# Kernel tuning notes

Measured on AMD Instinct MI355X. Metric: run time of the kernel, lower is better.

The kernel has to match this reference:

```python
import jax, jax.numpy as jnp
import numpy as np

N = 10000
E = 160000
NEG_SLOPE = 0.2
BN_EPS = 1e-5


def _gat_conv(x, W, a_src, a_dst, b, src, dst, n, heads):
    # PyG GATConv, concat=False (mean over heads), shared lin for src/dst.
    H = heads
    C = W.shape[1] // H
    h = (x @ W).reshape(n, H, C)                       # (N,H,C)
    e_s = jnp.einsum('nhc,hc->nh', h, a_src)           # (N,H)
    e_d = jnp.einsum('nhc,hc->nh', h, a_dst)
    alpha = jax.nn.leaky_relu(e_s[src] + e_d[dst], NEG_SLOPE)   # (E',H)
    amax = jax.ops.segment_max(alpha, dst, num_segments=n)       # per-dst softmax
    ex = jnp.exp(alpha - amax[dst])
    denom = jax.ops.segment_sum(ex, dst, num_segments=n)
    w = ex / (denom[dst] + 1e-16)
    out = jax.ops.segment_sum(h[src] * w[:, :, None], dst, num_segments=n)  # (N,H,C)
    return out.mean(axis=1) + b


def _bn(x, g, b):
    mu = x.mean(axis=0)
    var = x.var(axis=0)  # biased, as torch BN training forward
    return (x - mu) * jax.lax.rsqrt(var + BN_EPS) * g + b


def setup_inputs() -> dict:
    key = jax.random.key(0)
    ks = jax.random.split(key, 32)
    d = {}
    d['x'] = jax.random.normal(ks[0], (N, 64), jnp.float32)
    d['edge_index'] = jax.random.randint(ks[1], (2, E), 0, N, jnp.int64)
    s = lambda k, shape, fan: jax.random.normal(k, shape, jnp.float32) * (1.0 / np.sqrt(fan))
    d['Wp'] = s(ks[2], (64, 128), 64); d['bp'] = jnp.zeros((128,), jnp.float32)
    # conv0: 8 heads, per-head 128
    d['W0'] = s(ks[3], (128, 8 * 128), 128); d['as0'] = s(ks[4], (8, 128), 128)
    d['ad0'] = s(ks[5], (8, 128), 128); d['b0'] = jnp.zeros((128,), jnp.float32)
    d['g0'] = jnp.ones((128,), jnp.float32); d['be0'] = jnp.zeros((128,), jnp.float32)
    # conv1: same shape
    d['W1'] = s(ks[6], (128, 8 * 128), 128); d['as1'] = s(ks[7], (8, 128), 128)
    d['ad1'] = s(ks[8], (8, 128), 128); d['b1'] = jnp.zeros((128,), jnp.float32)
    d['g1'] = jnp.ones((128,), jnp.float32); d['be1'] = jnp.zeros((128,), jnp.float32)
    # conv2: 1 head, out 64
    d['W2'] = s(ks[9], (128, 64), 128); d['as2'] = s(ks[10], (1, 64), 64)
    d['ad2'] = s(ks[11], (1, 64), 64); d['b2'] = jnp.zeros((64,), jnp.float32)
    d['g2'] = jnp.ones((64,), jnp.float32); d['be2'] = jnp.zeros((64,), jnp.float32)
    # residual projection for layer 2 (128 -> 64)
    d['Wr'] = s(ks[12], (128, 64), 128); d['br'] = jnp.zeros((64,), jnp.float32)
    return d


def reference(x, edge_index, Wp, bp, W0, as0, ad0, b0, g0, be0,
              W1, as1, ad1, b1, g1, be1, W2, as2, ad2, b2, g2, be2, Wr, br):
    n = x.shape[0]
    loops = jnp.arange(n, dtype=edge_index.dtype)
    src = jnp.concatenate([edge_index[0], loops])  # add_self_loops=True
    dst = jnp.concatenate([edge_index[1], loops])
    h = x @ Wp + bp
    # layer 0 (8 heads, identity residual)
    hr = h
    h = jax.nn.elu(_bn(_gat_conv(h, W0, as0, ad0, b0, src, dst, n, 8), g0, be0)) + hr
    # layer 1
    hr = h
    h = jax.nn.elu(_bn(_gat_conv(h, W1, as1, ad1, b1, src, dst, n, 8), g1, be1)) + hr
    # layer 2 (1 head, linear residual 128->64)
    hr = h @ Wr + br
    h = jax.nn.elu(_bn(_gat_conv(h, W2, as2, ad2, b2, src, dst, n, 1), g2, be2)) + hr
    return h
```

## Files before the change

kernel.cpp:

```cpp
#include <hip/hip_runtime.h>
#include <hip/hip_bf16.h>
#include <cstdint>
#include <cstddef>

#define TPB 256

typedef __attribute__((ext_vector_type(8))) short bf16x8;
typedef __attribute__((ext_vector_type(8))) unsigned short ushort8;
typedef __attribute__((ext_vector_type(4))) float f32x4;

static __device__ __forceinline__ float bf2f(unsigned short u) {
  union { unsigned int i; float f; } c;
  c.i = ((unsigned int)u) << 16;
  return c.f;
}
static __device__ __forceinline__ unsigned short f2us(float v) {
  __hip_bfloat16 b = __float2bfloat16(v);
  return *(unsigned short*)&b;
}

__global__ void detect_kernel(const unsigned int* __restrict__ w, int* __restrict__ flag) {
  __shared__ int any32;
  if (threadIdx.x == 0) any32 = 0;
  __syncthreads();
  for (int i = threadIdx.x; i < 1024; i += TPB)
    if (w[2 * i + 1] != 0u) any32 = 1;
  __syncthreads();
  if (threadIdx.x == 0) *flag = any32;
}

__global__ void decode_kernel(const void* __restrict__ raw, const int* __restrict__ flag,
                              int* __restrict__ src, int* __restrict__ dst, int E, int n) {
  int i = blockIdx.x * TPB + threadIdx.x;
  int tot = E + n;
  if (i >= tot) return;
  if (i < E) {
    if (*flag) {
      const int* p = (const int*)raw;
      src[i] = p[i];
      dst[i] = p[E + i];
    } else {
      const long long* p = (const long long*)raw;
      src[i] = (int)p[i];
      dst[i] = (int)p[E + i];
    }
  } else {
    src[i] = i - E;
    dst[i] = i - E;
  }
}

__global__ void count_kernel(const int* __restrict__ dst, int* __restrict__ counts, int etot) {
  int i = blockIdx.x * TPB + threadIdx.x;
  if (i < etot) atomicAdd(&counts[dst[i]], 1);
}

__global__ void scan_kernel(const int* __restrict__ counts, int* __restrict__ row_ptr, int n) {
  __shared__ int part[TPB];
  int tid = threadIdx.x;
  int chunk = (n + TPB - 1) / TPB;
  int begin = tid * chunk;
  int end = begin + chunk; if (end > n) end = n;
  int s = 0;
  for (int i = begin; i < end && i < n; i++) s += counts[i];
  part[tid] = s;
  __syncthreads();
  for (int off = 1; off < TPB; off <<= 1) {
    int v = (tid >= off) ? part[tid - off] : 0;
    __syncthreads();
    part[tid] += v;
    __syncthreads();
  }
  int base = (tid == 0) ? 0 : part[tid - 1];
  for (int i = begin; i < end && i < n; i++) { row_ptr[i] = base; base += counts[i]; }
  if (tid == TPB - 1) row_ptr[n] = base;
}

__global__ void fill_kernel(const int* __restrict__ src, const int* __restrict__ dst,
                            const int* __restrict__ row_ptr, int* __restrict__ fill,
                            int* __restrict__ sorted_src, int etot) {
  int i = blockIdx.x * TPB + threadIdx.x;
  if (i >= etot) return;
  int d = dst[i];
  int pos = row_ptr[d] + atomicAdd(&fill[d], 1);
  sorted_src[pos] = src[i];
}

__global__ void f32_to_bf16_kernel(const float* __restrict__ in, __hip_bfloat16* __restrict__ out, int n) {
  int i = blockIdx.x * TPB + threadIdx.x;
  if (i < n) out[i] = __float2bfloat16(in[i]);
}

__global__ void f32_to_bf16_T_kernel(const float* __restrict__ in, __hip_bfloat16* __restrict__ out,
                                     int K, int N) {
  __shared__ float tile[32][33];
  const int k0 = blockIdx.x * 32, n0 = blockIdx.y * 32;
  const int tx = threadIdx.x & 31, ty = threadIdx.x >> 5;
  for (int r = ty; r < 32; r += 8) {
    int k = k0 + r, n = n0 + tx;
    tile[r][tx] = (k < K && n < N) ? in[(size_t)k * N + n] : 0.f;
  }
  __syncthreads();
  for (int r = ty; r < 32; r += 8) {
    int n = n0 + r, k = k0 + tx;
    if (n < N && k < K) out[(size_t)n * K + k] = __float2bfloat16(tile[tx][r]);
  }
}

__global__ __launch_bounds__(256) void gemm_bf16t_kernel(
    const short* __restrict__ A, const short* __restrict__ Bt,
    const float* __restrict__ bias, float* __restrict__ C,
    __hip_bfloat16* __restrict__ Cb, int M, int Ncols, int K,
    const float* __restrict__ asrc, const float* __restrict__ adst,
    float* __restrict__ es_out, float* __restrict__ ed_out, int H, int hshift) {
  __shared__ short As[64][40];
  __shared__ short Bs[128][40];

  const int tid = threadIdx.x;
  const int lane = tid & 63;
  const int w = tid >> 6;
  const int bm = blockIdx.x * 64;
  const int bn = blockIdx.y * 128;

  f32x4 acc[8];
#pragma unroll
  for (int nt = 0; nt < 8; nt++) acc[nt] = (f32x4){0.f, 0.f, 0.f, 0.f};

  const int arow = tid >> 2;
  const int akk = (tid & 3) << 3;
  const int brow = tid >> 1;
  const int bkk = (tid & 1) << 4;

  for (int k0 = 0; k0 < K; k0 += 32) {
    {
      int gr = bm + arow;
      if (gr < M) {
        *(bf16x8*)&As[arow][akk] = *(const bf16x8*)&A[(size_t)gr * K + k0 + akk];
      } else {
        bf16x8 z = {0, 0, 0, 0, 0, 0, 0, 0};
        *(bf16x8*)&As[arow][akk] = z;
      }
    }
    {
      int gbn = bn + brow;
      if (gbn < Ncols) {
        const short* bp = &Bt[(size_t)gbn * K + k0 + bkk];
        *(bf16x8*)&Bs[brow][bkk]     = *(const bf16x8*)bp;
        *(bf16x8*)&Bs[brow][bkk + 8] = *(const bf16x8*)(bp + 8);
      } else {
        bf16x8 z = {0, 0, 0, 0, 0, 0, 0, 0};
        *(bf16x8*)&Bs[brow][bkk] = z;
        *(bf16x8*)&Bs[brow][bkk + 8] = z;
      }
    }
    __syncthreads();

    bf16x8 a = *(const bf16x8*)&As[w * 16 + (lane & 15)][(lane >> 4) * 8];
#pragma unroll
    for (int nt = 0; nt < 8; nt++) {
      bf16x8 b = *(const bf16x8*)&Bs[nt * 16 + (lane & 15)][(lane >> 4) * 8];
      acc[nt] = __builtin_amdgcn_mfma_f32_16x16x32_bf16(a, b, acc[nt], 0, 0, 0);
    }
    __syncthreads();
  }

  float p1[4] = {0.f, 0.f, 0.f, 0.f};
  float p2[4] = {0.f, 0.f, 0.f, 0.f};

#pragma unroll
  for (int nt = 0; nt < 8; nt++) {
    int gc = bn + nt * 16 + (lane & 15);
    if (gc >= Ncols) continue;
    float bv = bias ? bias[gc] : 0.f;
    float asv = es_out ? asrc[gc] : 0.f;
    float adv = es_out ? adst[gc] : 0.f;
#pragma unroll
    for (int q = 0; q < 4; q++) {
      int gr = bm + w * 16 + (lane >> 4) * 4 + q;
      if (gr < M) {
        float val = acc[nt][q] + bv;
        if (C) C[(size_t)gr * Ncols + gc] = val;
        if (Cb) Cb[(size_t)gr * Ncols + gc] = __float2bfloat16(val);
        p1[q] += val * asv;
        p2[q] += val * adv;
      }
    }
  }

  if (es_out) {
    const int head = bn >> hshift;
#pragma unroll
    for (int q = 0; q < 4; q++) {
      float s1 = p1[q], s2 = p2[q];
      s1 += __shfl_xor(s1, 1); s2 += __shfl_xor(s2, 1);
      s1 += __shfl_xor(s1, 2); s2 += __shfl_xor(s2, 2);
      s1 += __shfl_xor(s1, 4); s2 += __shfl_xor(s2, 4);
      s1 += __shfl_xor(s1, 8); s2 += __shfl_xor(s2, 8);
      int gr = bm + w * 16 + (lane >> 4) * 4 + q;
      if ((lane & 15) == 0 && gr < M) {
        es_out[(size_t)gr * H + head] = s1;
        ed_out[(size_t)gr * H + head] = s2;
      }
    }
  }
}

__global__ __launch_bounds__(256) void gat_weights_kernel(
    const int* __restrict__ row_ptr, const int* __restrict__ srcs,
    const float* __restrict__ es, const float* __restrict__ ed,
    float* __restrict__ wbuf, int etot, int n) {
  const int wave = threadIdx.x >> 6, lane = threadIdx.x & 63;
  const int v = blockIdx.x * 4 + wave;
  if (v >= n) return;
  const int begin = row_ptr[v], deg = row_ptr[v + 1] - begin;
  const int eh = lane & 7, ee = lane >> 3;
  const float edv = ed[(size_t)v * 8 + eh];

  if (deg <= 64) {
    float a[8];
#pragma unroll
    for (int b = 0; b < 8; b++) {
      a[b] = -1e30f;
      int e = b * 8 + ee;
      if (e < deg) {
        int s = srcs[begin + e];
        float t = es[(size_t)s * 8 + eh] + edv;
        a[b] = t > 0.f ? t : 0.2f * t;
      }
    }
    float m = a[0];
#pragma unroll
    for (int b = 1; b < 8; b++) m = fmaxf(m, a[b]);
    m = fmaxf(m, __shfl_xor(m, 8));
    m = fmaxf(m, __shfl_xor(m, 16));
    m = fmaxf(m, __shfl_xor(m, 32));
    float dsum = 0.f;
#pragma unroll
    for (int b = 0; b < 8; b++) { a[b] = __expf(a[b] - m); dsum += a[b]; }
    dsum += __shfl_xor(dsum, 8);
    dsum += __shfl_xor(dsum, 16);
    dsum += __shfl_xor(dsum, 32);
    const float invd = 1.0f / (dsum + 1e-16f);
#pragma unroll
    for (int b = 0; b < 8; b++) {
      int e = b * 8 + ee;
      if (e < deg) wbuf[(size_t)eh * etot + begin + e] = a[b] * invd;
    }
  } else {
    float m = -1e30f;
    for (int e = ee; e < deg; e += 8) {
      int s = srcs[begin + e];
      float t = es[(size_t)s * 8 + eh] + edv;
      t = t > 0.f ? t : 0.2f * t;
      m = fmaxf(m, t);
    }
    m = fmaxf(m, __shfl_xor(m, 8));
    m = fmaxf(m, __shfl_xor(m, 16));
    m = fmaxf(m, __shfl_xor(m, 32));
    float dsum = 0.f;
    for (int e = ee; e < deg; e += 8) {
      int s = srcs[begin + e];
      float t = es[(size_t)s * 8 + eh] + edv;
      t = t > 0.f ? t : 0.2f * t;
      dsum += __expf(t - m);
    }
    dsum += __shfl_xor(dsum, 8);
    dsum += __shfl_xor(dsum, 16);
    dsum += __shfl_xor(dsum, 32);
    const float invd = 1.0f / (dsum + 1e-16f);
    for (int e = ee; e < deg; e += 8) {
      int s = srcs[begin + e];
      float t = es[(size_t)s * 8 + eh] + edv;
      t = t > 0.f ? t : 0.2f * t;
      wbuf[(size_t)eh * etot + begin + e] = __expf(t - m) * invd;
    }
  }
}

__global__ __launch_bounds__(256) void gat_gather_head_kernel(
    const int* __restrict__ row_ptr, const int* __restrict__ srcs,
    const unsigned short* __restrict__ gb, const float* __restrict__ wbuf,
    unsigned short* __restrict__ partial, int etot, int n, int nb) {
  const int h = blockIdx.x & 7;
  const int nblk = blockIdx.x >> 3;
  const int wave = threadIdx.x >> 6, lane = threadIdx.x & 63;

  __shared__ float wlds[4][64];
  __shared__ int slds[4][64];

  const int per = (n + nb - 1) / nb;
  const int v1 = min((nblk + 1) * per, n);
  const float* wb = wbuf + (size_t)h * etot;
  const unsigned short* gsl = gb + h * 128;
  unsigned short* pout = partial + (size_t)h * n * 128;
  const int g = lane >> 4;
  const int c8 = (lane & 15) * 8;

  for (int v = nblk * per + wave; v < v1; v += 4) {
    const int begin = row_ptr[v];
    const int deg = row_ptr[v + 1] - begin;
    float acc[8];
#pragma unroll
    for (int k = 0; k < 8; k++) acc[k] = 0.f;

    for (int base = 0; base < deg; base += 64) {
      const int cnt = min(64, deg - base);
      int sv = 0; float wv = 0.f;
      if (lane < cnt) {
        sv = srcs[begin + base + lane];
        wv = wb[begin + base + lane];
      }
      slds[wave][lane] = sv;
      wlds[wave][lane] = wv;
      const int npad = (cnt + 15) & ~15;
      for (int j0 = 0; j0 < npad; j0 += 16) {
        int s0 = slds[wave][j0 + g];
        int s1 = slds[wave][j0 + 4 + g];
        int s2 = slds[wave][j0 + 8 + g];
        int s3 = slds[wave][j0 + 12 + g];
        float w0 = wlds[wave][j0 + g];
        float w1 = wlds[wave][j0 + 4 + g];
        float w2 = wlds[wave][j0 + 8 + g];
        float w3 = wlds[wave][j0 + 12 + g];
        ushort8 u0 = *(const ushort8*)&gsl[(size_t)s0 * 1024 + c8];
        ushort8 u1 = *(const ushort8*)&gsl[(size_t)s1 * 1024 + c8];
        ushort8 u2 = *(const ushort8*)&gsl[(size_t)s2 * 1024 + c8];
        ushort8 u3 = *(const ushort8*)&gsl[(size_t)s3 * 1024 + c8];
#pragma unroll
        for (int k = 0; k < 8; k++) {
          acc[k] += w0 * bf2f(u0[k]) + w1 * bf2f(u1[k])
                  + w2 * bf2f(u2[k]) + w3 * bf2f(u3[k]);
        }
      }
    }

#pragma unroll
    for (int k = 0; k < 8; k++) {
      acc[k] += __shfl_xor(acc[k], 16);
      acc[k] += __shfl_xor(acc[k], 32);
    }
    if (lane < 16) {
      unsigned int o[4];
#pragma unroll
      for (int k = 0; k < 4; k++)
        o[k] = (unsigned int)f2us(acc[2 * k]) | ((unsigned int)f2us(acc[2 * k + 1]) << 16);
      *(uint4*)&pout[(size_t)v * 128 + c8] = *(uint4*)o;
    }
  }
}

__global__ __launch_bounds__(256) void gat_reduce_bn_kernel(
    const unsigned short* __restrict__ partial, const float* __restrict__ bias,
    float* __restrict__ out, float* __restrict__ sums, int n) {
  const int t = threadIdx.x;
  const int stride = gridDim.x * TPB;
  float s0 = 0.f, q0 = 0.f, s1 = 0.f, q1 = 0.f;
  for (int idx = blockIdx.x * TPB + t; idx < n * 64; idx += stride) {
    int v = idx >> 6, c = (idx & 63) * 2;
    float sx = 0.f, sy = 0.f;
#pragma unroll
    for (int h = 0; h < 8; h++) {
      unsigned int u = *(const unsigned int*)&partial[(size_t)h * n * 128 + (size_t)v * 128 + c];
      sx += bf2f((unsigned short)u);
      sy += bf2f((unsigned short)(u >> 16));
    }
    float x0 = sx * 0.125f + bias[c];
    float x1 = sy * 0.125f + bias[c + 1];
    out[(size_t)v * 128 + c]     = x0;
    out[(size_t)v * 128 + c + 1] = x1;
    s0 += x0; q0 += x0 * x0;
    s1 += x1; q1 += x1 * x1;
  }
  __shared__ float ls0[TPB], lq0[TPB], ls1[TPB], lq1[TPB];
  ls0[t] = s0; lq0[t] = q0; ls1[t] = s1; lq1[t] = q1;
  __syncthreads();
  if (t < 64) {
    float S0 = ls0[t] + ls0[t + 64] + ls0[t + 128] + ls0[t + 192];
    float Q0 = lq0[t] + lq0[t + 64] + lq0[t + 128] + lq0[t + 192];
    float S1 = ls1[t] + ls1[t + 64] + ls1[t + 128] + ls1[t + 192];
    float Q1 = lq1[t] + lq1[t + 64] + lq1[t + 128] + lq1[t + 192];
    int c = t * 2;
    atomicAdd(&sums[c], S0);
    atomicAdd(&sums[128 + c], Q0);
    atomicAdd(&sums[c + 1], S1);
    atomicAdd(&sums[128 + c + 1], Q1);
  }
}

__global__ __launch_bounds__(256) void gat_aggregate1_kernel(
    const int* __restrict__ row_ptr, const int* __restrict__ srcs,
    const float* __restrict__ g, const float* __restrict__ es,
    const float* __restrict__ ed, const float* __restrict__ bias,
    float* __restrict__ out, int n) {
  const int wave = threadIdx.x >> 6;
  const int lane = threadIdx.x & 63;
  const int v = blockIdx.x * 4 + wave;

  __shared__ float wlds[4][64];
  __shared__ int slds[4][64];

  if (v >= n) return;

  const int begin = row_ptr[v];
  const int deg = row_ptr[v + 1] - begin;
  const float edv = ed[v];

  float acc = 0.f;

  if (deg <= 64) {
    float a = -1e30f;
    int s = 0;
    if (lane < deg) {
      s = srcs[begin + lane];
      float t = es[s] + edv;
      a = t > 0.f ? t : 0.2f * t;
    }
    float m = a;
#pragma unroll
    for (int off = 32; off > 0; off >>= 1) m = fmaxf(m, __shfl_xor(m, off));
    float p = __expf(a - m);
    float dsum = p;
#pragma unroll
    for (int off = 32; off > 0; off >>= 1) dsum += __shfl_xor(dsum, off);
    const float invd = 1.0f / (dsum + 1e-16f);
    wlds[wave][lane] = p * invd;
    slds[wave][lane] = s;

    const int npad = (deg + 7) & ~7;
    for (int j0 = 0; j0 < npad; j0 += 8) {
      float w0 = wlds[wave][j0 + 0], w1 = wlds[wave][j0 + 1];
      float w2 = wlds[wave][j0 + 2], w3 = wlds[wave][j0 + 3];
      float w4 = wlds[wave][j0 + 4], w5 = wlds[wave][j0 + 5];
      float w6 = wlds[wave][j0 + 6], w7 = wlds[wave][j0 + 7];
      int s0 = slds[wave][j0 + 0], s1 = slds[wave][j0 + 1];
      int s2 = slds[wave][j0 + 2], s3 = slds[wave][j0 + 3];
      int s4 = slds[wave][j0 + 4], s5 = slds[wave][j0 + 5];
      int s6 = slds[wave][j0 + 6], s7 = slds[wave][j0 + 7];
      float f0 = g[(size_t)s0 * 64 + lane];
      float f1 = g[(size_t)s1 * 64 + lane];
      float f2 = g[(size_t)s2 * 64 + lane];
      float f3 = g[(size_t)s3 * 64 + lane];
      float f4 = g[(size_t)s4 * 64 + lane];
      float f5 = g[(size_t)s5 * 64 + lane];
      float f6 = g[(size_t)s6 * 64 + lane];
      float f7 = g[(size_t)s7 * 64 + lane];
      acc += (w0 * f0 + w1 * f1) + (w2 * f2 + w3 * f3)
           + (w4 * f4 + w5 * f5) + (w6 * f6 + w7 * f7);
    }
  } else {
    float pm = -1e30f;
    for (int j = lane; j < deg; j += 64) {
      float a = es[srcs[begin + j]] + edv;
      a = a > 0.f ? a : 0.2f * a;
      pm = fmaxf(pm, a);
    }
#pragma unroll
    for (int off = 32; off > 0; off >>= 1) pm = fmaxf(pm, __shfl_xor(pm, off));
    float ps = 0.f;
    for (int j = lane; j < deg; j += 64) {
      float a = es[srcs[begin + j]] + edv;
      a = a > 0.f ? a : 0.2f * a;
      ps += __expf(a - pm);
    }
#pragma unroll
    for (int off = 32; off > 0; off >>= 1) ps += __shfl_xor(ps, off);
    const float invd = 1.0f / (ps + 1e-16f);

    for (int base = 0; base < deg; base += 64) {
      int cnt = min(64, deg - base);
      float wv = 0.f; int s = 0;
      if (lane < cnt) {
        s = srcs[begin + base + lane];
        float a = es[s] + edv;
        a = a > 0.f ? a : 0.2f * a;
        wv = __expf(a - pm) * invd;
      }
      wlds[wave][lane] = wv;
      slds[wave][lane] = s;
      const int npad = (cnt + 7) & ~7;
      for (int j0 = 0; j0 < npad; j0 += 8) {
        float w0 = wlds[wave][j0 + 0], w1 = wlds[wave][j0 + 1];
        float w2 = wlds[wave][j0 + 2], w3 = wlds[wave][j0 + 3];
        float w4 = wlds[wave][j0 + 4], w5 = wlds[wave][j0 + 5];
        float w6 = wlds[wave][j0 + 6], w7 = wlds[wave][j0 + 7];
        int s0 = slds[wave][j0 + 0], s1 = slds[wave][j0 + 1];
        int s2 = slds[wave][j0 + 2], s3 = slds[wave][j0 + 3];
        int s4 = slds[wave][j0 + 4], s5 = slds[wave][j0 + 5];
        int s6 = slds[wave][j0 + 6], s7 = slds[wave][j0 + 7];
        float f0 = g[(size_t)s0 * 64 + lane];
        float f1 = g[(size_t)s1 * 64 + lane];
        float f2 = g[(size_t)s2 * 64 + lane];
        float f3 = g[(size_t)s3 * 64 + lane];
        float f4 = g[(size_t)s4 * 64 + lane];
        float f5 = g[(size_t)s5 * 64 + lane];
        float f6 = g[(size_t)s6 * 64 + lane];
        float f7 = g[(size_t)s7 * 64 + lane];
        acc += (w0 * f0 + w1 * f1) + (w2 * f2 + w3 * f3)
             + (w4 * f4 + w5 * f5) + (w6 * f6 + w7 * f7);
      }
    }
  }
  out[(size_t)v * 64 + lane] = acc + bias[lane];
}

template <int C>
__global__ void bn_stats_kernel(const float* __restrict__ x, int n, float* __restrict__ sums) {
  constexpr int T = 256;
  constexpr int RPI = T / C;
  constexpr int ITER = 8;
  constexpr int ROWS = RPI * ITER;
  int c = threadIdx.x % C;
  int r0 = threadIdx.x / C;
  int rowBase = blockIdx.x * ROWS;
  float s = 0.f, q = 0.f;
  for (int it = 0; it < ITER; ++it) {
    int r = rowBase + it * RPI + r0;
    if (r < n) {
      float v = x[(size_t)r * C + c];
      s += v; q += v * v;
    }
  }
  __shared__ float ls[T], lq[T];
  ls[threadIdx.x] = s; lq[threadIdx.x] = q;
  __syncthreads();
  if (threadIdx.x < C) {
    float ts = 0.f, tq = 0.f;
    for (int r = 0; r < RPI; ++r) { ts += ls[c + r * C]; tq += lq[c + r * C]; }
    atomicAdd(&sums[c], ts);
    atomicAdd(&sums[C + c], tq);
  }
}

template <int C>
__global__ void bn_elu_res_kernel(const float* __restrict__ x, const float* __restrict__ sums,
                                  const float* __restrict__ gamma, const float* __restrict__ beta,
                                  const float* __restrict__ res, float* __restrict__ out,
                                  __hip_bfloat16* __restrict__ outb, int n) {
  int i = blockIdx.x * TPB + threadIdx.x;
  if (i >= n * C) return;
  int c = i % C;
  float inv_n = 1.0f / (float)n;
  float mu = sums[c] * inv_n;
  float var = sums[C + c] * inv_n - mu * mu;
  float y = (x[i] - mu) * rsqrtf(var + 1e-5f) * gamma[c] + beta[c];
  y = y > 0.f ? y : expm1f(y);
  y += res[i];
  out[i] = y;
  if (outb) outb[i] = __float2bfloat16(y);
}

extern "C" void kernel_launch(void* const* d_in, const int* in_sizes, int n_in,
                              void* d_out, int out_size, void* d_ws, size_t ws_size,
                              hipStream_t stream) {
  const float* x   = (const float*)d_in[0];
  const void*  ei  = d_in[1];
  const float* Wp  = (const float*)d_in[2];
  const float* bp  = (const float*)d_in[3];
  const float* W0  = (const float*)d_in[4];
  const float* as0 = (const float*)d_in[5];
  const float* ad0 = (const float*)d_in[6];
  const float* b0  = (const float*)d_in[7];
  const float* g0  = (const float*)d_in[8];
  const float* be0 = (const float*)d_in[9];
  const float* W1  = (const float*)d_in[10];
  const float* as1 = (const float*)d_in[11];
  const float* ad1 = (const float*)d_in[12];
  const float* b1  = (const float*)d_in[13];
  const float* g1  = (const float*)d_in[14];
  const float* be1 = (const float*)d_in[15];
  const float* W2  = (const float*)d_in[16];
  const float* as2 = (const float*)d_in[17];
  const float* ad2 = (const float*)d_in[18];
  const float* b2  = (const float*)d_in[19];
  const float* g2  = (const float*)d_in[20];
  const float* be2 = (const float*)d_in[21];
  const float* Wr  = (const float*)d_in[22];
  const float* br  = (const float*)d_in[23];

  const int N = in_sizes[0] / 64;
  const int E = in_sizes[1] / 2;
  const int ETOT = E + N;

  char* wsp = (char*)d_ws;
  size_t off = 0;
  auto alloc = [&](size_t bytes) -> void* {
    void* p = wsp + off;
    off += (bytes + 255) & ~(size_t)255;
    return p;
  };
  int*   flag    = (int*)alloc(4);
  int*   e_src   = (int*)alloc((size_t)ETOT * 4);
  int*   e_dst   = (int*)alloc((size_t)ETOT * 4);
  int*   counts  = (int*)alloc((size_t)N * 4);
  int*   fillc   = (int*)alloc((size_t)N * 4);
  int*   row_ptr = (int*)alloc((size_t)(N + 1) * 4);
  int*   s_src   = (int*)alloc((size_t)ETOT * 4);
  float* hA      = (float*)alloc((size_t)N * 128 * 4);
  float* hB      = (float*)alloc((size_t)N * 128 * 4);
  float* gat     = (float*)alloc((size_t)N * 128 * 4);
  float* es      = (float*)alloc((size_t)N * 8 * 4);
  float* ed      = (float*)alloc((size_t)N * 8 * 4);
  float* bnsum   = (float*)alloc(2 * 128 * 4);
  float* wbuf    = (float*)alloc((size_t)ETOT * 8 * 4);
  __hip_bfloat16* gbufb = (__hip_bfloat16*)alloc((size_t)N * 1024 * 2);
  float* gbuf    = (float*)gbufb;
  unsigned short* partial = (unsigned short*)alloc((size_t)N * 1024 * 2);
  __hip_bfloat16* xb  = (__hip_bfloat16*)alloc((size_t)N * 64 * 2);
  __hip_bfloat16* hAb = (__hip_bfloat16*)alloc((size_t)N * 128 * 2);
  __hip_bfloat16* hBb = (__hip_bfloat16*)alloc((size_t)N * 128 * 2);
  __hip_bfloat16* WpT = (__hip_bfloat16*)alloc((size_t)128 * 64 * 2);
  __hip_bfloat16* W0T = (__hip_bfloat16*)alloc((size_t)1024 * 128 * 2);
  __hip_bfloat16* W1T = (__hip_bfloat16*)alloc((size_t)1024 * 128 * 2);
  __hip_bfloat16* W2T = (__hip_bfloat16*)alloc((size_t)64 * 128 * 2);
  __hip_bfloat16* WrT = (__hip_bfloat16*)alloc((size_t)64 * 128 * 2);

  const int egrid = (ETOT + TPB - 1) / TPB;
  const int mgrid = (N + 63) / 64;
  const int NB = 512;
  auto cgrid = [](int n) { return (n + TPB - 1) / TPB; };

  detect_kernel<<<1, TPB, 0, stream>>>((const unsigned int*)ei, flag);
  decode_kernel<<<egrid, TPB, 0, stream>>>(ei, flag, e_src, e_dst, E, N);
  hipMemsetAsync(counts, 0, (size_t)N * 4, stream);
  hipMemsetAsync(fillc, 0, (size_t)N * 4, stream);
  count_kernel<<<egrid, TPB, 0, stream>>>(e_dst, counts, ETOT);
  scan_kernel<<<1, TPB, 0, stream>>>(counts, row_ptr, N);
  fill_kernel<<<egrid, TPB, 0, stream>>>(e_src, e_dst, row_ptr, fillc, s_src, ETOT);

  f32_to_bf16_kernel<<<cgrid(N * 64), TPB, 0, stream>>>(x, xb, N * 64);
  f32_to_bf16_T_kernel<<<dim3(2, 4), 256, 0, stream>>>(Wp, WpT, 64, 128);
  f32_to_bf16_T_kernel<<<dim3(4, 32), 256, 0, stream>>>(W0, W0T, 128, 1024);
  f32_to_bf16_T_kernel<<<dim3(4, 32), 256, 0, stream>>>(W1, W1T, 128, 1024);
  f32_to_bf16_T_kernel<<<dim3(4, 2), 256, 0, stream>>>(W2, W2T, 128, 64);
  f32_to_bf16_T_kernel<<<dim3(4, 2), 256, 0, stream>>>(Wr, WrT, 128, 64);

  gemm_bf16t_kernel<<<dim3(mgrid, 1), 256, 0, stream>>>(
      (const short*)xb, (const short*)WpT, bp, hA, hAb, N, 128, 64,
      nullptr, nullptr, nullptr, nullptr, 1, 7);

  gemm_bf16t_kernel<<<dim3(mgrid, 8), 256, 0, stream>>>(
      (const short*)hAb, (const short*)W0T, nullptr, nullptr, gbufb, N, 1024, 128,
      as0, ad0, es, ed, 8, 7);
  gat_weights_kernel<<<(N + 3) / 4, 256, 0, stream>>>(row_ptr, s_src, es, ed, wbuf, ETOT, N);
  gat_gather_head_kernel<<<8 * NB, 256, 0, stream>>>(
      row_ptr, s_src, (const unsigned short*)gbufb, wbuf, partial, ETOT, N, NB);
  hipMemsetAsync(bnsum, 0, 2 * 128 * 4, stream);
  gat_reduce_bn_kernel<<<512, 256, 0, stream>>>(partial, b0, gat, bnsum, N);
  bn_elu_res_kernel<128><<<cgrid(N * 128), TPB, 0, stream>>>(gat, bnsum, g0, be0, hA, hB, hBb, N);

  gemm_bf16t_kernel<<<dim3(mgrid, 8), 256, 0, stream>>>(
      (const short*)hBb, (const short*)W1T, nullptr, nullptr, gbufb, N, 1024, 128,
      as1, ad1, es, ed, 8, 7);
  gat_weights_kernel<<<(N + 3) / 4, 256, 0, stream>>>(row_ptr, s_src, es, ed, wbuf, ETOT, N);
  gat_gather_head_kernel<<<8 * NB, 256, 0, stream>>>(
      row_ptr, s_src, (const unsigned short*)gbufb, wbuf, partial, ETOT, N, NB);
  hipMemsetAsync(bnsum, 0, 2 * 128 * 4, stream);
  gat_reduce_bn_kernel<<<512, 256, 0, stream>>>(partial, b1, gat, bnsum, N);
  bn_elu_res_kernel<128><<<cgrid(N * 128), TPB, 0, stream>>>(gat, bnsum, g1, be1, hB, hA, hAb, N);

  gemm_bf16t_kernel<<<dim3(mgrid, 1), 256, 0, stream>>>(
      (const short*)hAb, (const short*)WrT, br, hB, nullptr, N, 64, 128,
      nullptr, nullptr, nullptr, nullptr, 1, 7);
  gemm_bf16t_kernel<<<dim3(mgrid, 1), 256, 0, stream>>>(
      (const short*)hAb, (const short*)W2T, nullptr, gbuf, nullptr, N, 64, 128,
      as2, ad2, es, ed, 1, 6);
  gat_aggregate1_kernel<<<(N + 3) / 4, 256, 0, stream>>>(row_ptr, s_src, gbuf, es, ed, b2, gat, N);
  hipMemsetAsync(bnsum, 0, 2 * 64 * 4, stream);
  bn_stats_kernel<64><<<(N + 31) / 32, 256, 0, stream>>>(gat, N, bnsum);
  bn_elu_res_kernel<64><<<cgrid(N * 64), TPB, 0, stream>>>(gat, bnsum, g2, be2, hB, (float*)d_out, nullptr, N);
}
```

Baseline: 312.4 us.

## Fuse GAT softmax into gather, merge small kernels and layer-2 GEMMs

The separate attention-weight kernel is removed: per-edge softmax weights are now computed inside the head gather kernel, so the edge-by-head weight buffer is never written to or read back from global memory. Setup kernels are merged: detect, memset and count fold into prep and decode-count kernels, and the five weight-transpose launches become one. The layer-2 residual projection and conv2 GEMM are combined into a single 128-wide GEMM, BN stats are folded into the aggregate kernel, and the bnsum memsets move into the GEMM. The softmax logits are recomputed in the gather for each edge, and in the high-degree path they are recomputed twice.

```diff
diff --git a/kernel.cpp b/kernel.cpp
--- a/kernel.cpp
+++ b/kernel.cpp
@@ -19,40 +19,41 @@
   return *(unsigned short*)&b;
 }
 
-__global__ void detect_kernel(const unsigned int* __restrict__ w, int* __restrict__ flag) {
-  __shared__ int any32;
-  if (threadIdx.x == 0) any32 = 0;
-  __syncthreads();
-  for (int i = threadIdx.x; i < 1024; i += TPB)
-    if (w[2 * i + 1] != 0u) any32 = 1;
-  __syncthreads();
-  if (threadIdx.x == 0) *flag = any32;
-}
-
-__global__ void decode_kernel(const void* __restrict__ raw, const int* __restrict__ flag,
-                              int* __restrict__ src, int* __restrict__ dst, int E, int n) {
+__global__ void prep_kernel(const unsigned int* __restrict__ ei, int* __restrict__ flag,
+                            int* __restrict__ counts, int* __restrict__ fillc, int n) {
+  int i = blockIdx.x * TPB + threadIdx.x;
+  if (i < n) { counts[i] = 0; fillc[i] = 0; }
+  if (blockIdx.x == 0) {
+    __shared__ int any32;
+    if (threadIdx.x == 0) any32 = 0;
+    __syncthreads();
+    for (int k = threadIdx.x; k < 1024; k += TPB)
+      if (ei[2 * k + 1] != 0u) any32 = 1;
+    __syncthreads();
+    if (threadIdx.x == 0) *flag = any32;
+  }
+}
+
+__global__ void decode_count_kernel(const void* __restrict__ raw, const int* __restrict__ flag,
+                                    int* __restrict__ src, int* __restrict__ dst,
+                                    int* __restrict__ counts, int E, int n) {
   int i = blockIdx.x * TPB + threadIdx.x;
   int tot = E + n;
   if (i >= tot) return;
+  int s, d;
   if (i < E) {
     if (*flag) {
       const int* p = (const int*)raw;
-      src[i] = p[i];
-      dst[i] = p[E + i];
+      s = p[i]; d = p[E + i];
     } else {
       const long long* p = (const long long*)raw;
-      src[i] = (int)p[i];
-      dst[i] = (int)p[E + i];
+      s = (int)p[i]; d = (int)p[E + i];
     }
   } else {
-    src[i] = i - E;
-    dst[i] = i - E;
-  }
-}
-
-__global__ void count_kernel(const int* __restrict__ dst, int* __restrict__ counts, int etot) {
-  int i = blockIdx.x * TPB + threadIdx.x;
-  if (i < etot) atomicAdd(&counts[dst[i]], 1);
+    s = i - E; d = i - E;
+  }
+  src[i] = s; dst[i] = d;
+  atomicAdd(&counts[d], 1);
 }
 
 __global__ void scan_kernel(const int* __restrict__ counts, int* __restrict__ row_ptr, int n) {
@@ -91,19 +92,43 @@
   if (i < n) out[i] = __float2bfloat16(in[i]);
 }
 
-__global__ void f32_to_bf16_T_kernel(const float* __restrict__ in, __hip_bfloat16* __restrict__ out,
-                                     int K, int N) {
+__global__ void convert_weights_kernel(
+    const float* __restrict__ Wp, const float* __restrict__ W0,
+    const float* __restrict__ W1, const float* __restrict__ W2,
+    const float* __restrict__ Wr, const float* __restrict__ as2,
+    const float* __restrict__ ad2, const float* __restrict__ br,
+    __hip_bfloat16* __restrict__ WpT, __hip_bfloat16* __restrict__ W0T,
+    __hip_bfloat16* __restrict__ W1T, __hip_bfloat16* __restrict__ WrW2T,
+    float* __restrict__ asrc_c, float* __restrict__ adst_c, float* __restrict__ bias_c) {
+  const int b = blockIdx.x;
+  if (b == 280) {
+    int t = threadIdx.x;
+    if (t < 128) {
+      asrc_c[t] = (t < 64) ? 0.f : as2[t - 64];
+      adst_c[t] = (t < 64) ? 0.f : ad2[t - 64];
+      bias_c[t] = (t < 64) ? br[t] : 0.f;
+    }
+    return;
+  }
+  const float* src; __hip_bfloat16* dst; int K, N, t;
+  if (b < 8)        { src = Wp; dst = WpT; K = 64;  N = 128;  t = b; }
+  else if (b < 136) { src = W0; dst = W0T; K = 128; N = 1024; t = b - 8; }
+  else if (b < 264) { src = W1; dst = W1T; K = 128; N = 1024; t = b - 136; }
+  else if (b < 272) { src = W2; dst = WrW2T + 64 * 128; K = 128; N = 64; t = b - 264; }
+  else              { src = Wr; dst = WrW2T;            K = 128; N = 64; t = b - 272; }
+
   __shared__ float tile[32][33];
-  const int k0 = blockIdx.x * 32, n0 = blockIdx.y * 32;
+  const int kt = (K + 31) / 32;
+  const int k0 = (t % kt) * 32, n0 = (t / kt) * 32;
   const int tx = threadIdx.x & 31, ty = threadIdx.x >> 5;
   for (int r = ty; r < 32; r += 8) {
     int k = k0 + r, n = n0 + tx;
-    tile[r][tx] = (k < K && n < N) ? in[(size_t)k * N + n] : 0.f;
+    tile[r][tx] = (k < K && n < N) ? src[(size_t)k * N + n] : 0.f;
   }
   __syncthreads();
   for (int r = ty; r < 32; r += 8) {
     int n = n0 + r, k = k0 + tx;
-    if (n < N && k < K) out[(size_t)n * K + k] = __float2bfloat16(tile[tx][r]);
+    if (n < N && k < K) dst[(size_t)n * K + k] = __float2bfloat16(tile[tx][r]);
   }
 }
 
@@ -112,11 +137,14 @@
     const float* __restrict__ bias, float* __restrict__ C,
     __hip_bfloat16* __restrict__ Cb, int M, int Ncols, int K,
     const float* __restrict__ asrc, const float* __restrict__ adst,
-    float* __restrict__ es_out, float* __restrict__ ed_out, int H, int hshift) {
+    float* __restrict__ es_out, float* __restrict__ ed_out, int H, int hshift,
+    float* __restrict__ bn_zero, int bn_len) {
   __shared__ short As[64][40];
   __shared__ short Bs[128][40];
 
   const int tid = threadIdx.x;
+  if (bn_zero && blockIdx.x == 0 && blockIdx.y == 0 && tid < bn_len) bn_zero[tid] = 0.f;
+
   const int lane = tid & 63;
   const int w = tid >> 6;
   const int bm = blockIdx.x * 64;
@@ -205,82 +233,11 @@
   }
 }
 
-__global__ __launch_bounds__(256) void gat_weights_kernel(
-    const int* __restrict__ row_ptr, const int* __restrict__ srcs,
-    const float* __restrict__ es, const float* __restrict__ ed,
-    float* __restrict__ wbuf, int etot, int n) {
-  const int wave = threadIdx.x >> 6, lane = threadIdx.x & 63;
-  const int v = blockIdx.x * 4 + wave;
-  if (v >= n) return;
-  const int begin = row_ptr[v], deg = row_ptr[v + 1] - begin;
-  const int eh = lane & 7, ee = lane >> 3;
-  const float edv = ed[(size_t)v * 8 + eh];
-
-  if (deg <= 64) {
-    float a[8];
-#pragma unroll
-    for (int b = 0; b < 8; b++) {
-      a[b] = -1e30f;
-      int e = b * 8 + ee;
-      if (e < deg) {
-        int s = srcs[begin + e];
-        float t = es[(size_t)s * 8 + eh] + edv;
-        a[b] = t > 0.f ? t : 0.2f * t;
-      }
-    }
-    float m = a[0];
-#pragma unroll
-    for (int b = 1; b < 8; b++) m = fmaxf(m, a[b]);
-    m = fmaxf(m, __shfl_xor(m, 8));
-    m = fmaxf(m, __shfl_xor(m, 16));
-    m = fmaxf(m, __shfl_xor(m, 32));
-    float dsum = 0.f;
-#pragma unroll
-    for (int b = 0; b < 8; b++) { a[b] = __expf(a[b] - m); dsum += a[b]; }
-    dsum += __shfl_xor(dsum, 8);
-    dsum += __shfl_xor(dsum, 16);
-    dsum += __shfl_xor(dsum, 32);
-    const float invd = 1.0f / (dsum + 1e-16f);
-#pragma unroll
-    for (int b = 0; b < 8; b++) {
-      int e = b * 8 + ee;
-      if (e < deg) wbuf[(size_t)eh * etot + begin + e] = a[b] * invd;
-    }
-  } else {
-    float m = -1e30f;
-    for (int e = ee; e < deg; e += 8) {
-      int s = srcs[begin + e];
-      float t = es[(size_t)s * 8 + eh] + edv;
-      t = t > 0.f ? t : 0.2f * t;
-      m = fmaxf(m, t);
-    }
-    m = fmaxf(m, __shfl_xor(m, 8));
-    m = fmaxf(m, __shfl_xor(m, 16));
-    m = fmaxf(m, __shfl_xor(m, 32));
-    float dsum = 0.f;
-    for (int e = ee; e < deg; e += 8) {
-      int s = srcs[begin + e];
-      float t = es[(size_t)s * 8 + eh] + edv;
-      t = t > 0.f ? t : 0.2f * t;
-      dsum += __expf(t - m);
-    }
-    dsum += __shfl_xor(dsum, 8);
-    dsum += __shfl_xor(dsum, 16);
-    dsum += __shfl_xor(dsum, 32);
-    const float invd = 1.0f / (dsum + 1e-16f);
-    for (int e = ee; e < deg; e += 8) {
-      int s = srcs[begin + e];
-      float t = es[(size_t)s * 8 + eh] + edv;
-      t = t > 0.f ? t : 0.2f * t;
-      wbuf[(size_t)eh * etot + begin + e] = __expf(t - m) * invd;
-    }
-  }
-}
-
 __global__ __launch_bounds__(256) void gat_gather_head_kernel(
     const int* __restrict__ row_ptr, const int* __restrict__ srcs,
-    const unsigned short* __restrict__ gb, const float* __restrict__ wbuf,
-    unsigned short* __restrict__ partial, int etot, int n, int nb) {
+    const unsigned short* __restrict__ gb, const float* __restrict__ es,
+    const float* __restrict__ ed, unsigned short* __restrict__ partial,
+    int n, int nb) {
   const int h = blockIdx.x & 7;
   const int nblk = blockIdx.x >> 3;
   const int wave = threadIdx.x >> 6, lane = threadIdx.x & 63;
@@ -290,7 +247,6 @@
 
   const int per = (n + nb - 1) / nb;
   const int v1 = min((nblk + 1) * per, n);
-  const float* wb = wbuf + (size_t)h * etot;
   const unsigned short* gsl = gb + h * 128;
   unsigned short* pout = partial + (size_t)h * n * 128;
   const int g = lane >> 4;
@@ -299,20 +255,29 @@
   for (int v = nblk * per + wave; v < v1; v += 4) {
     const int begin = row_ptr[v];
     const int deg = row_ptr[v + 1] - begin;
+    const float edv = ed[(size_t)v * 8 + h];
     float acc[8];
 #pragma unroll
     for (int k = 0; k < 8; k++) acc[k] = 0.f;
 
-    for (int base = 0; base < deg; base += 64) {
-      const int cnt = min(64, deg - base);
-      int sv = 0; float wv = 0.f;
-      if (lane < cnt) {
-        sv = srcs[begin + base + lane];
-        wv = wb[begin + base + lane];
-      }
+    if (deg <= 64) {
+      int sv = 0; float a = -1e30f;
+      if (lane < deg) {
+        sv = srcs[begin + lane];
+        float t = es[(size_t)sv * 8 + h] + edv;
+        a = t > 0.f ? t : 0.2f * t;
+      }
+      float m = a;
+#pragma unroll
+      for (int off = 32; off > 0; off >>= 1) m = fmaxf(m, __shfl_xor(m, off));
+      float p = __expf(a - m);
+      float ds = p;
+#pragma unroll
+      for (int off = 32; off > 0; off >>= 1) ds += __shfl_xor(ds, off);
       slds[wave][lane] = sv;
-      wlds[wave][lane] = wv;
-      const int npad = (cnt + 15) & ~15;
+      wlds[wave][lane] = p * (1.0f / (ds + 1e-16f));
+
+      const int npad = (deg + 15) & ~15;
       for (int j0 = 0; j0 < npad; j0 += 16) {
         int s0 = slds[wave][j0 + g];
         int s1 = slds[wave][j0 + 4 + g];
@@ -332,6 +297,63 @@
                   + w2 * bf2f(u2[k]) + w3 * bf2f(u3[k]);
         }
       }
+    } else {
+      float m = -1e30f;
+      for (int base = 0; base < deg; base += 64) {
+        if (base + lane < deg) {
+          int s = srcs[begin + base + lane];
+          float t = es[(size_t)s * 8 + h] + edv;
+          t = t > 0.f ? t : 0.2f * t;
+          m = fmaxf(m, t);
+        }
+      }
+#pragma unroll
+      for (int off = 32; off > 0; off >>= 1) m = fmaxf(m, __shfl_xor(m, off));
+      float ds = 0.f;
+      for (int base = 0; base < deg; base += 64) {
+        if (base + lane < deg) {
+          int s = srcs[begin + base + lane];
+          float t = es[(size_t)s * 8 + h] + edv;
+          t = t > 0.f ? t : 0.2f * t;
+          ds += __expf(t - m);
+        }
+      }
+#pragma unroll
+      for (int off = 32; off > 0; off >>= 1) ds += __shfl_xor(ds, off);
+      const float invd = 1.0f / (ds + 1e-16f);
+
+      for (int base = 0; base < deg; base += 64) {
+        const int cnt = min(64, deg - base);
+        int sv = 0; float wv = 0.f;
+        if (lane < cnt) {
+          sv = srcs[begin + base + lane];
+          float t = es[(size_t)sv * 8 + h] + edv;
+          t = t > 0.f ? t : 0.2f * t;
+          wv = __expf(t - m) * invd;
+        }
+        slds[wave][lane] = sv;
+        wlds[wave][lane] = wv;
+        const int npad = (cnt + 15) & ~15;
+        for (int j0 = 0; j0 < npad; j0 += 16) {
+          int s0 = slds[wave][j0 + g];
+          int s1 = slds[wave][j0 + 4 + g];
+          int s2 = slds[wave][j0 + 8 + g];
+          int s3 = slds[wave][j0 + 12 + g];
+          float w0 = wlds[wave][j0 + g];
+          float w1 = wlds[wave][j0 + 4 + g];
+          float w2 = wlds[wave][j0 + 8 + g];
+          float w3 = wlds[wave][j0 + 12 + g];
+          ushort8 u0 = *(const ushort8*)&gsl[(size_t)s0 * 1024 + c8];
+          ushort8 u1 = *(const ushort8*)&gsl[(size_t)s1 * 1024 + c8];
+          ushort8 u2 = *(const ushort8*)&gsl[(size_t)s2 * 1024 + c8];
+          ushort8 u3 = *(const ushort8*)&gsl[(size_t)s3 * 1024 + c8];
+#pragma unroll
+          for (int k = 0; k < 8; k++) {
+            acc[k] += w0 * bf2f(u0[k]) + w1 * bf2f(u1[k])
+                    + w2 * bf2f(u2[k]) + w3 * bf2f(u3[k]);
+          }
+        }
+      }
     }
 
 #pragma unroll
@@ -389,95 +411,45 @@
 
 __global__ __launch_bounds__(256) void gat_aggregate1_kernel(
     const int* __restrict__ row_ptr, const int* __restrict__ srcs,
-    const float* __restrict__ g, const float* __restrict__ es,
+    const float* __restrict__ g, int gstride, const float* __restrict__ es,
     const float* __restrict__ ed, const float* __restrict__ bias,
-    float* __restrict__ out, int n) {
+    float* __restrict__ out, float* __restrict__ sums, int n) {
   const int wave = threadIdx.x >> 6;
   const int lane = threadIdx.x & 63;
   const int v = blockIdx.x * 4 + wave;
+  const bool act = (v < n);
 
   __shared__ float wlds[4][64];
   __shared__ int slds[4][64];
-
-  if (v >= n) return;
-
-  const int begin = row_ptr[v];
-  const int deg = row_ptr[v + 1] - begin;
-  const float edv = ed[v];
-
-  float acc = 0.f;
-
-  if (deg <= 64) {
-    float a = -1e30f;
-    int s = 0;
-    if (lane < deg) {
-      s = srcs[begin + lane];
-      float t = es[s] + edv;
-      a = t > 0.f ? t : 0.2f * t;
-    }
-    float m = a;
-#pragma unroll
-    for (int off = 32; off > 0; off >>= 1) m = fmaxf(m, __shfl_xor(m, off));
-    float p = __expf(a - m);
-    float dsum = p;
-#pragma unroll
-    for (int off = 32; off > 0; off >>= 1) dsum += __shfl_xor(dsum, off);
-    const float invd = 1.0f / (dsum + 1e-16f);
-    wlds[wave][lane] = p * invd;
-    slds[wave][lane] = s;
-
-    const int npad = (deg + 7) & ~7;
-    for (int j0 = 0; j0 < npad; j0 += 8) {
-      float w0 = wlds[wave][j0 + 0], w1 = wlds[wave][j0 + 1];
-      float w2 = wlds[wave][j0 + 2], w3 = wlds[wave][j0 + 3];
-      float w4 = wlds[wave][j0 + 4], w5 = wlds[wave][j0 + 5];
-      float w6 = wlds[wave][j0 + 6], w7 = wlds[wave][j0 + 7];
-      int s0 = slds[wave][j0 + 0], s1 = slds[wave][j0 + 1];
-      int s2 = slds[wave][j0 + 2], s3 = slds[wave][j0 + 3];
-      int s4 = slds[wave][j0 + 4], s5 = slds[wave][j0 + 5];
-      int s6 = slds[wave][j0 + 6], s7 = slds[wave][j0 + 7];
-      float f0 = g[(size_t)s0 * 64 + lane];
-      float f1 = g[(size_t)s1 * 64 + lane];
-      float f2 = g[(size_t)s2 * 64 + lane];
-      float f3 = g[(size_t)s3 * 64 + lane];
-      float f4 = g[(size_t)s4 * 64 + lane];
-      float f5 = g[(size_t)s5 * 64 + lane];
-      float f6 = g[(size_t)s6 * 64 + lane];
-      float f7 = g[(size_t)s7 * 64 + lane];
-      acc += (w0 * f0 + w1 * f1) + (w2 * f2 + w3 * f3)
-           + (w4 * f4 + w5 * f5) + (w6 * f6 + w7 * f7);
-    }
-  } else {
-    float pm = -1e30f;
-    for (int j = lane; j < deg; j += 64) {
-      float a = es[srcs[begin + j]] + edv;
-      a = a > 0.f ? a : 0.2f * a;
-      pm = fmaxf(pm, a);
-    }
-#pragma unroll
-    for (int off = 32; off > 0; off >>= 1) pm = fmaxf(pm, __shfl_xor(pm, off));
-    float ps = 0.f;
-    for (int j = lane; j < deg; j += 64) {
-      float a = es[srcs[begin + j]] + edv;
-      a = a > 0.f ? a : 0.2f * a;
-      ps += __expf(a - pm);
-    }
-#pragma unroll
-    for (int off = 32; off > 0; off >>= 1) ps += __shfl_xor(ps, off);
-    const float invd = 1.0f / (ps + 1e-16f);
-
-    for (int base = 0; base < deg; base += 64) {
-      int cnt = min(64, deg - base);
-      float wv = 0.f; int s = 0;
-      if (lane < cnt) {
-        s = srcs[begin + base + lane];
-        float a = es[s] + edv;
-        a = a > 0.f ? a : 0.2f * a;
-        wv = __expf(a - pm) * invd;
-      }
-      wlds[wave][lane] = wv;
+  __shared__ float ls[TPB], lq[TPB];
+
+  float result = 0.f;
+  if (act) {
+    const int begin = row_ptr[v];
+    const int deg = row_ptr[v + 1] - begin;
+    const float edv = ed[v];
+    float acc = 0.f;
+
+    if (deg <= 64) {
+      float a = -1e30f;
+      int s = 0;
+      if (lane < deg) {
+        s = srcs[begin + lane];
+        float t = es[s] + edv;
+        a = t > 0.f ? t : 0.2f * t;
+      }
+      float m = a;
+#pragma unroll
+      for (int off = 32; off > 0; off >>= 1) m = fmaxf(m, __shfl_xor(m, off));
+      float p = __expf(a - m);
+      float dsum = p;
+#pragma unroll
+      for (int off = 32; off > 0; off >>= 1) dsum += __shfl_xor(dsum, off);
+      const float invd = 1.0f / (dsum + 1e-16f);
+      wlds[wave][lane] = p * invd;
       slds[wave][lane] = s;
-      const int npad = (cnt + 7) & ~7;
+
+      const int npad = (deg + 7) & ~7;
       for (int j0 = 0; j0 < npad; j0 += 8) {
         float w0 = wlds[wave][j0 + 0], w1 = wlds[wave][j0 + 1];
         float w2 = wlds[wave][j0 + 2], w3 = wlds[wave][j0 + 3];
@@ -487,55 +459,90 @@
         int s2 = slds[wave][j0 + 2], s3 = slds[wave][j0 + 3];
         int s4 = slds[wave][j0 + 4], s5 = slds[wave][j0 + 5];
         int s6 = slds[wave][j0 + 6], s7 = slds[wave][j0 + 7];
-        float f0 = g[(size_t)s0 * 64 + lane];
-        float f1 = g[(size_t)s1 * 64 + lane];
-        float f2 = g[(size_t)s2 * 64 + lane];
-        float f3 = g[(size_t)s3 * 64 + lane];
-        float f4 = g[(size_t)s4 * 64 + lane];
-        float f5 = g[(size_t)s5 * 64 + lane];
-        float f6 = g[(size_t)s6 * 64 + lane];
-        float f7 = g[(size_t)s7 * 64 + lane];
+        float f0 = g[(size_t)s0 * gstride + lane];
+        float f1 = g[(size_t)s1 * gstride + lane];
+        float f2 = g[(size_t)s2 * gstride + lane];
+        float f3 = g[(size_t)s3 * gstride + lane];
+        float f4 = g[(size_t)s4 * gstride + lane];
+        float f5 = g[(size_t)s5 * gstride + lane];
+        float f6 = g[(size_t)s6 * gstride + lane];
+        float f7 = g[(size_t)s7 * gstride + lane];
         acc += (w0 * f0 + w1 * f1) + (w2 * f2 + w3 * f3)
              + (w4 * f4 + w5 * f5) + (w6 * f6 + w7 * f7);
       }
-    }
-  }
-  out[(size_t)v * 64 + lane] = acc + bias[lane];
-}
-
-template <int C>
-__global__ void bn_stats_kernel(const float* __restrict__ x, int n, float* __restrict__ sums) {
-  constexpr int T = 256;
-  constexpr int RPI = T / C;
-  constexpr int ITER = 8;
-  constexpr int ROWS = RPI * ITER;
-  int c = threadIdx.x % C;
-  int r0 = threadIdx.x / C;
-  int rowBase = blockIdx.x * ROWS;
-  float s = 0.f, q = 0.f;
-  for (int it = 0; it < ITER; ++it) {
-    int r = rowBase + it * RPI + r0;
-    if (r < n) {
-      float v = x[(size_t)r * C + c];
-      s += v; q += v * v;
-    }
-  }
-  __shared__ float ls[T], lq[T];
-  ls[threadIdx.x] = s; lq[threadIdx.x] = q;
+    } else {
+      float pm = -1e30f;
+      for (int j = lane; j < deg; j += 64) {
+        float a = es[srcs[begin + j]] + edv;
+        a = a > 0.f ? a : 0.2f * a;
+        pm = fmaxf(pm, a);
+      }
+#pragma unroll
+      for (int off = 32; off > 0; off >>= 1) pm = fmaxf(pm, __shfl_xor(pm, off));
+      float ps = 0.f;
+      for (int j = lane; j < deg; j += 64) {
+        float a = es[srcs[begin + j]] + edv;
+        a = a > 0.f ? a : 0.2f * a;
+        ps += __expf(a - pm);
+      }
+#pragma unroll
+      for (int off = 32; off > 0; off >>= 1) ps += __shfl_xor(ps, off);
+      const float invd = 1.0f / (ps + 1e-16f);
+
+      for (int base = 0; base < deg; base += 64) {
+        int cnt = min(64, deg - base);
+        float wv = 0.f; int s = 0;
+        if (lane < cnt) {
+          s = srcs[begin + base + lane];
+          float a = es[s] + edv;
+          a = a > 0.f ? a : 0.2f * a;
+          wv = __expf(a - pm) * invd;
+        }
+        wlds[wave][lane] = wv;
+        slds[wave][lane] = s;
+        const int npad = (cnt + 7) & ~7;
+        for (int j0 = 0; j0 < npad; j0 += 8) {
+          float w0 = wlds[wave][j0 + 0], w1 = wlds[wave][j0 + 1];
+          float w2 = wlds[wave][j0 + 2], w3 = wlds[wave][j0 + 3];
+          float w4 = wlds[wave][j0 + 4], w5 = wlds[wave][j0 + 5];
+          float w6 = wlds[wave][j0 + 6], w7 = wlds[wave][j0 + 7];
+          int s0 = slds[wave][j0 + 0], s1 = slds[wave][j0 + 1];
+          int s2 = slds[wave][j0 + 2], s3 = slds[wave][j0 + 3];
+          int s4 = slds[wave][j0 + 4], s5 = slds[wave][j0 + 5];
+          int s6 = slds[wave][j0 + 6], s7 = slds[wave][j0 + 7];
+          float f0 = g[(size_t)s0 * gstride + lane];
+          float f1 = g[(size_t)s1 * gstride + lane];
+          float f2 = g[(size_t)s2 * gstride + lane];
+          float f3 = g[(size_t)s3 * gstride + lane];
+          float f4 = g[(size_t)s4 * gstride + lane];
+          float f5 = g[(size_t)s5 * gstride + lane];
+          float f6 = g[(size_t)s6 * gstride + lane];
+          float f7 = g[(size_t)s7 * gstride + lane];
+          acc += (w0 * f0 + w1 * f1) + (w2 * f2 + w3 * f3)
+               + (w4 * f4 + w5 * f5) + (w6 * f6 + w7 * f7);
+        }
+      }
+    }
+    result = acc + bias[lane];
+    out[(size_t)v * 64 + lane] = result;
+  }
+
+  ls[threadIdx.x] = act ? result : 0.f;
+  lq[threadIdx.x] = act ? result * result : 0.f;
   __syncthreads();
-  if (threadIdx.x < C) {
-    float ts = 0.f, tq = 0.f;
-    for (int r = 0; r < RPI; ++r) { ts += ls[c + r * C]; tq += lq[c + r * C]; }
-    atomicAdd(&sums[c], ts);
-    atomicAdd(&sums[C + c], tq);
+  if (threadIdx.x < 64) {
+    float S = ls[threadIdx.x] + ls[threadIdx.x + 64] + ls[threadIdx.x + 128] + ls[threadIdx.x + 192];
+    float Q = lq[threadIdx.x] + lq[threadIdx.x + 64] + lq[threadIdx.x + 128] + lq[threadIdx.x + 192];
+    atomicAdd(&sums[threadIdx.x], S);
+    atomicAdd(&sums[64 + threadIdx.x], Q);
   }
 }
 
 template <int C>
 __global__ void bn_elu_res_kernel(const float* __restrict__ x, const float* __restrict__ sums,
                                   const float* __restrict__ gamma, const float* __restrict__ beta,
-                                  const float* __restrict__ res, float* __restrict__ out,
-                                  __hip_bfloat16* __restrict__ outb, int n) {
+                                  const float* __restrict__ res, int res_stride,
+                                  float* __restrict__ out, __hip_bfloat16* __restrict__ outb, int n) {
   int i = blockIdx.x * TPB + threadIdx.x;
   if (i >= n * C) return;
   int c = i % C;
@@ -544,7 +551,7 @@
   float var = sums[C + c] * inv_n - mu * mu;
   float y = (x[i] - mu) * rsqrtf(var + 1e-5f) * gamma[c] + beta[c];
   y = y > 0.f ? y : expm1f(y);
-  y += res[i];
+  y += res[(size_t)(i / C) * res_stride + c];
   out[i] = y;
   if (outb) outb[i] = __float2bfloat16(y);
 }
@@ -601,9 +608,11 @@
   float* es      = (float*)alloc((size_t)N * 8 * 4);
   float* ed      = (float*)alloc((size_t)N * 8 * 4);
   float* bnsum   = (float*)alloc(2 * 128 * 4);
-  float* wbuf    = (float*)alloc((size_t)ETOT * 8 * 4);
+  float* asrc_c  = (float*)alloc(128 * 4);
+  float* adst_c  = (float*)alloc(128 * 4);
+  float* bias_c  = (float*)alloc(128 * 4);
   __hip_bfloat16* gbufb = (__hip_bfloat16*)alloc((size_t)N * 1024 * 2);
-  float* gbuf    = (float*)gbufb;
+  float* comb    = (float*)gbufb;
   unsigned short* partial = (unsigned short*)alloc((size_t)N * 1024 * 2);
   __hip_bfloat16* xb  = (__hip_bfloat16*)alloc((size_t)N * 64 * 2);
   __hip_bfloat16* hAb = (__hip_bfloat16*)alloc((size_t)N * 128 * 2);
@@ -611,61 +620,49 @@
   __hip_bfloat16* WpT = (__hip_bfloat16*)alloc((size_t)128 * 64 * 2);
   __hip_bfloat16* W0T = (__hip_bfloat16*)alloc((size_t)1024 * 128 * 2);
   __hip_bfloat16* W1T = (__hip_bfloat16*)alloc((size_t)1024 * 128 * 2);
-  __hip_bfloat16* W2T = (__hip_bfloat16*)alloc((size_t)64 * 128 * 2);
-  __hip_bfloat16* WrT = (__hip_bfloat16*)alloc((size_t)64 * 128 * 2);
+  __hip_bfloat16* WrW2T = (__hip_bfloat16*)alloc((size_t)128 * 128 * 2);
 
   const int egrid = (ETOT + TPB - 1) / TPB;
   const int mgrid = (N + 63) / 64;
   const int NB = 512;
   auto cgrid = [](int n) { return (n + TPB - 1) / TPB; };
 
-  detect_kernel<<<1, TPB, 0, stream>>>((const unsigned int*)ei, flag);
-  decode_kernel<<<egrid, TPB, 0, stream>>>(ei, flag, e_src, e_dst, E, N);
-  hipMemsetAsync(counts, 0, (size_t)N * 4, stream);
-  hipMemsetAsync(fillc, 0, (size_t)N * 4, stream);
-  count_kernel<<<egrid, TPB, 0, stream>>>(e_dst, counts, ETOT);
+  prep_kernel<<<cgrid(N), TPB, 0, stream>>>((const unsigned int*)ei, flag, counts, fillc, N);
+  decode_count_kernel<<<egrid, TPB, 0, stream>>>(ei, flag, e_src, e_dst, counts, E, N);
   scan_kernel<<<1, TPB, 0, stream>>>(counts, row_ptr, N);
   fill_kernel<<<egrid, TPB, 0, stream>>>(e_src, e_dst, row_ptr, fillc, s_src, ETOT);
 
   f32_to_bf16_kernel<<<cgrid(N * 64), TPB, 0, stream>>>(x, xb, N * 64);
-  f32_to_bf16_T_kernel<<<dim3(2, 4), 256, 0, stream>>>(Wp, WpT, 64, 128);
-  f32_to_bf16_T_kernel<<<dim3(4, 32), 256, 0, stream>>>(W0, W0T, 128, 1024);
-  f32_to_bf16_T_kernel<<<dim3(4, 32), 256, 0, stream>>>(W1, W1T, 128, 1024);
-  f32_to_bf16_T_kernel<<<dim3(4, 2), 256, 0, stream>>>(W2, W2T, 128, 64);
-  f32_to_bf16_T_kernel<<<dim3(4, 2), 256, 0, stream>>>(Wr, WrT, 128, 64);
+  convert_weights_kernel<<<281, 256, 0, stream>>>(
+      Wp, W0, W1, W2, Wr, as2, ad2, br, WpT, W0T, W1T, WrW2T, asrc_c, adst_c, bias_c);
 
   gemm_bf16t_kernel<<<dim3(mgrid, 1), 256, 0, stream>>>(
       (const short*)xb, (const short*)WpT, bp, hA, hAb, N, 128, 64,
-      nullptr, nullptr, nullptr, nullptr, 1, 7);
+      nullptr, nullptr, nullptr, nullptr, 1, 7, nullptr, 0);
 
   gemm_bf16t_kernel<<<dim3(mgrid, 8), 256, 0, stream>>>(
       (const short*)hAb, (const short*)W0T, nullptr, nullptr, gbufb, N, 1024, 128,
-      as0, ad0, es, ed, 8, 7);
-  gat_weights_kernel<<<(N + 3) / 4, 256, 0, stream>>>(row_ptr, s_src, es, ed, wbuf, ETOT, N);
+      as0, ad0, es, ed, 8, 7, bnsum, 256);
   gat_gather_head_kernel<<<8 * NB, 256, 0, stream>>>(
-      row_ptr, s_src, (const unsigned short*)gbufb, wbuf, partial, ETOT, N, NB);
-  hipMemsetAsync(bnsum, 0, 2 * 128 * 4, stream);
+      row_ptr, s_src, (const unsigned short*)gbufb, es, ed, partial, N, NB);
   gat_reduce_bn_kernel<<<512, 256, 0, stream>>>(partial, b0, gat, bnsum, N);
-  bn_elu_res_kernel<128><<<cgrid(N * 128), TPB, 0, stream>>>(gat, bnsum, g0, be0, hA, hB, hBb, N);
+  bn_elu_res_kernel<128><<<cgrid(N * 128), TPB, 0, stream>>>(
+      gat, bnsum, g0, be0, hA, 128, hB, hBb, N);
 
   gemm_bf16t_kernel<<<dim3(mgrid, 8), 256, 0, stream>>>(
       (const short*)hBb, (const short*)W1T, nullptr, nullptr, gbufb, N, 1024, 128,
-      as1, ad1, es, ed, 8, 7);
-  gat_weights_kernel<<<(N + 3) / 4, 256, 0, stream>>>(row_ptr, s_src, es, ed, wbuf, ETOT, N);
+      as1, ad1, es, ed, 8, 7, bnsum, 256);
   gat_gather_head_kernel<<<8 * NB, 256, 0, stream>>>(
-      row_ptr, s_src, (const unsigned short*)gbufb, wbuf, partial, ETOT, N, NB);
-  hipMemsetAsync(bnsum, 0, 2 * 128 * 4, stream);
+      row_ptr, s_src, (const unsigned short*)gbufb, es, ed, partial, N, NB);
   gat_reduce_bn_kernel<<<512, 256, 0, stream>>>(partial, b1, gat, bnsum, N);
-  bn_elu_res_kernel<128><<<cgrid(N * 128), TPB, 0, stream>>>(gat, bnsum, g1, be1, hB, hA, hAb, N);
+  bn_elu_res_kernel<128><<<cgrid(N * 128), TPB, 0, stream>>>(
+      gat, bnsum, g1, be1, hB, 128, hA, hAb, N);
 
   gemm_bf16t_kernel<<<dim3(mgrid, 1), 256, 0, stream>>>(
-      (const short*)hAb, (const short*)WrT, br, hB, nullptr, N, 64, 128,
-      nullptr, nullptr, nullptr, nullptr, 1, 7);
-  gemm_bf16t_kernel<<<dim3(mgrid, 1), 256, 0, stream>>>(
-      (const short*)hAb, (const short*)W2T, nullptr, gbuf, nullptr, N, 64, 128,
-      as2, ad2, es, ed, 1, 6);
-  gat_aggregate1_kernel<<<(N + 3) / 4, 256, 0, stream>>>(row_ptr, s_src, gbuf, es, ed, b2, gat, N);
-  hipMemsetAsync(bnsum, 0, 2 * 64 * 4, stream);
-  bn_stats_kernel<64><<<(N + 31) / 32, 256, 0, stream>>>(gat, N, bnsum);
-  bn_elu_res_kernel<64><<<cgrid(N * 64), TPB, 0, stream>>>(gat, bnsum, g2, be2, hB, (float*)d_out, nullptr, N);
-}
+      (const short*)hAb, (const short*)WrW2T, bias_c, comb, nullptr, N, 128, 128,
+      asrc_c, adst_c, es, ed, 1, 7, bnsum, 128);
+  gat_aggregate1_kernel<<<(N + 3) / 4, 256, 0, stream>>>(
+      row_ptr, s_src, comb + 64, 128, es, ed, b2, gat, bnsum, N);
+  bn_elu_res_kernel<64><<<cgrid(N * 64), TPB, 0, stream>>>(
+      gat, bnsum, g2, be2, comb, 128, (float*)d_out, nullptr, N);
+}
```

After: 340.9 us. 9.1% more time.
